# Kernel optimization log

Hardware: AMD Instinct MI355X
Metric: run time of the kernel (lower is better)

Reference implementation:

```python
import jax, jax.numpy as jnp
import numpy as np

N_NODES = 50000
N_EDGES = 600000
LATENT = 128
STEPS = 4
BN_EPS = 1e-5


def _bn(h, gamma, beta):
    # BatchNorm1d in training mode: batch statistics over the row dim (biased var)
    mean = jnp.mean(h, axis=0)
    var = jnp.var(h, axis=0)
    return gamma * (h - mean) * jax.lax.rsqrt(var + BN_EPS) + beta


def setup_inputs() -> dict:
    key = jax.random.key(0)
    ks = jax.random.split(key, 9)
    L, S = LATENT, STEPS
    d = {}
    d["x"] = jax.random.normal(ks[0], (N_NODES, L), dtype=jnp.float32)
    d["edge_attr"] = jax.random.normal(ks[1], (N_EDGES, L), dtype=jnp.float32)
    d["edge_index"] = jax.random.randint(ks[2], (2, N_EDGES), 0, N_NODES, dtype=jnp.int64)
    # MLP weights: small init (BN normalizes hidden activations anyway)
    d["edge_W1"] = jax.random.normal(ks[3], (S, 3 * L, L), dtype=jnp.float32) * (1.0 / np.sqrt(3 * L))
    d["edge_b1"] = jnp.zeros((S, L), jnp.float32)
    d["edge_g1"] = jnp.ones((S, L), jnp.float32)
    d["edge_be1"] = jnp.zeros((S, L), jnp.float32)
    d["edge_W2"] = jax.random.normal(ks[4], (S, L, L), dtype=jnp.float32) * (1.0 / np.sqrt(L))
    d["edge_b2"] = jnp.zeros((S, L), jnp.float32)
    d["node_W1"] = jax.random.normal(ks[5], (S, 2 * L, L), dtype=jnp.float32) * (1.0 / np.sqrt(2 * L))
    d["node_b1"] = jnp.zeros((S, L), jnp.float32)
    d["node_g1"] = jnp.ones((S, L), jnp.float32)
    d["node_be1"] = jnp.zeros((S, L), jnp.float32)
    d["node_W2"] = jax.random.normal(ks[6], (S, L, L), dtype=jnp.float32) * (1.0 / np.sqrt(L))
    d["node_b2"] = jnp.zeros((S, L), jnp.float32)
    return d


def reference(x, edge_attr, edge_index, edge_W1, edge_b1, edge_g1, edge_be1,
              edge_W2, edge_b2, node_W1, node_b1, node_g1, node_be1,
              node_W2, node_b2):
    src = edge_index[0]  # x_j (source)
    dst = edge_index[1]  # x_i (target), also the scatter target
    for s in range(STEPS):
        # --- edge update (message) ---
        m = jnp.concatenate([x[dst], x[src], edge_attr], axis=1)  # [E, 3L]
        h = _bn(m @ edge_W1[s] + edge_b1[s], edge_g1[s], edge_be1[s])
        h = jax.nn.relu(h)
        h = jax.nn.relu(h @ edge_W2[s] + edge_b2[s])
        edge_attr = h + edge_attr  # residual
        # --- aggregate: scatter-sum to target nodes ---
        agg = jax.ops.segment_sum(edge_attr, dst, num_segments=N_NODES)  # [N, L]
        # --- node update ---
        n = jnp.concatenate([x, agg], axis=1)  # [N, 2L]
        h = _bn(n @ node_W1[s] + node_b1[s], node_g1[s], node_be1[s])
        h = jax.nn.relu(h)
        h = jax.nn.relu(h @ node_W2[s] + node_b2[s])
        x = h + x  # residual
    return x, edge_attr
```

## Files before the change

### kernel.cpp

```cpp
#include <hip/hip_runtime.h>
#include <hip/hip_bf16.h>
#include <cstdint>
#include <cstddef>

#define E_N 600000
#define NND 50000
#define L 128

typedef unsigned short u16;
typedef unsigned int u32;
typedef __attribute__((ext_vector_type(8))) short bf16x8;
typedef __attribute__((ext_vector_type(4))) float f32x4;

static __device__ __forceinline__ u16 f2bf(float f) {
  union { float f; u32 u; } c; c.f = f;
  return (u16)((c.u + 0x7fffu + ((c.u >> 16) & 1u)) >> 16);
}
static __device__ __forceinline__ u32 pk2(float a, float b) {
  return (u32)f2bf(a) | ((u32)f2bf(b) << 16);
}
static __device__ __forceinline__ float bf2f(u32 h) {
  union { u32 u; float f; } c; c.u = (h & 0xffffu) << 16; return c.f;
}
static __device__ __forceinline__ void atomAddF(float* p, float v) {
#if defined(__HIP_DEVICE_COMPILE__)
  unsafeAtomicAdd(p, v);
#else
  atomicAdd(p, v);
#endif
}
static __device__ __forceinline__ bf16x8 pack8(float4 a, float4 b) {
  union { bf16x8 v; u32 w[4]; } r;
  r.w[0] = pk2(a.x, a.y); r.w[1] = pk2(a.z, a.w);
  r.w[2] = pk2(b.x, b.y); r.w[3] = pk2(b.z, b.w);
  return r.v;
}
static __device__ __forceinline__ bf16x8 bnrelu8(bf16x8 raw, float4 sca, float4 scb,
                                                 float4 sha, float4 shb) {
  union { bf16x8 v; u16 h[8]; } in; in.v = raw;
  const float sc[8] = {sca.x, sca.y, sca.z, sca.w, scb.x, scb.y, scb.z, scb.w};
  const float sh[8] = {sha.x, sha.y, sha.z, sha.w, shb.x, shb.y, shb.z, shb.w};
  float f[8];
  #pragma unroll
  for (int i = 0; i < 8; ++i) f[i] = fmaxf(bf2f(in.h[i]) * sc[i] + sh[i], 0.f);
  union { bf16x8 v; u32 w[4]; } r;
  #pragma unroll
  for (int i = 0; i < 4; ++i) r.w[i] = pk2(f[2 * i], f[2 * i + 1]);
  return r.v;
}

#define MFMA(a, bfr, c) __builtin_amdgcn_mfma_f32_16x16x32_bf16((a), (bfr), (c), 0, 0, 0)

struct Stg { uint4 v[4]; };
template <int KF>
static __device__ __forceinline__ void stageLoad(const u16* __restrict__ Wt, int kc, int tid, Stg& s) {
  #pragma unroll
  for (int i = 0; i < 4; ++i) {
    const int slot = tid + i * 256;
    const int n = slot >> 3, kq = slot & 7;
    s.v[i] = *(const uint4*)(Wt + (size_t)n * KF + kc * 64 + kq * 8);
  }
}
static __device__ __forceinline__ void stageWrite(char* BsB, int tid, const Stg& s) {
  #pragma unroll
  for (int i = 0; i < 4; ++i) {
    const int slot = tid + i * 256;
    const int n = slot >> 3, kq = slot & 7;
    *(uint4*)(BsB + ((n * 128 + kq * 16) ^ ((n & 7) << 4))) = s.v[i];
  }
}
static __device__ __forceinline__ void chunkMFMA(const char* BsB, int wc, int l15, int lq,
                                                 const bf16x8 (&af)[2][2], f32x4 (&acc)[2][4]) {
  #pragma unroll
  for (int k2 = 0; k2 < 2; ++k2) {
    #pragma unroll
    for (int n = 0; n < 4; ++n) {
      const int col = wc * 64 + n * 16 + l15;
      const bf16x8 bfr = *(const bf16x8*)(BsB + ((col * 128 + k2 * 64 + lq * 16) ^ ((col & 7) << 4)));
      acc[0][n] = MFMA(af[0][k2], bfr, acc[0][n]);
      acc[1][n] = MFMA(af[1][k2], bfr, acc[1][n]);
    }
  }
}

__global__ __launch_bounds__(256) void k_cvt4(const float* __restrict__ in,
                                              u16* __restrict__ out, int n4) {
  const int i = blockIdx.x * 256 + threadIdx.x;
  if (i < n4) {
    const float4 v = *(const float4*)(in + (size_t)i * 4);
    uint2 o; o.x = pk2(v.x, v.y); o.y = pk2(v.z, v.w);
    *(uint2*)(out + (size_t)i * 4) = o;
  }
}

__global__ void k_wt(const float* __restrict__ W, u16* __restrict__ Wt, int K) {
  const int idx = blockIdx.x * 256 + threadIdx.x;
  const int total = 4 * K * 128;
  if (idx >= total) return;
  const int s = idx / (K * 128);
  const int rem = idx - s * K * 128;
  const int n = rem / K;
  const int k = rem - n * K;
  Wt[idx] = f2bf(W[(size_t)s * K * 128 + (size_t)k * 128 + n]);
}

__global__ void k_hist(const int* __restrict__ dstI, int* __restrict__ cnt) {
  const int i = blockIdx.x * 256 + threadIdx.x;
  if (i < E_N) atomicAdd(&cnt[dstI[i]], 1);
}

__global__ __launch_bounds__(1024) void k_scan(const int* __restrict__ cnt, int* __restrict__ startA) {
  __shared__ int buf[1024];
  __shared__ int carry;
  const int tid = threadIdx.x;
  if (tid == 0) carry = 0;
  __syncthreads();
  for (int base = 0; base < NND; base += 1024) {
    int v = (base + tid < NND) ? cnt[base + tid] : 0;
    buf[tid] = v;
    __syncthreads();
    for (int off = 1; off < 1024; off <<= 1) {
      int t = (tid >= off) ? buf[tid - off] : 0;
      __syncthreads();
      buf[tid] += t;
      __syncthreads();
    }
    const int incl = buf[tid];
    const int c = carry;
    if (base + tid < NND) startA[base + tid] = c + incl - v;
    __syncthreads();
    if (tid == 1023) carry = c + incl;
    __syncthreads();
  }
  if (tid == 0) startA[NND] = carry;
}

__global__ void k_fill(const int* __restrict__ dstI, const int* __restrict__ startA,
                       int* __restrict__ cur, int* __restrict__ eids) {
  const int i = blockIdx.x * 256 + threadIdx.x;
  if (i < E_N) {
    const int d = dstI[i];
    const int pos = atomicAdd(&cur[d], 1);
    eids[startA[d] + pos] = i;
  }
}

__global__ void k_perm(const int* __restrict__ srcI, const int* __restrict__ dstI,
                       const int* __restrict__ perm,
                       int* __restrict__ srcP, int* __restrict__ dstP) {
  const int i = blockIdx.x * 256 + threadIdx.x;
  if (i < E_N) {
    const int e = perm[i];
    srcP[i] = srcI[e];
    dstP[i] = dstI[e];
  }
}

__global__ __launch_bounds__(256) void k_agg(const u16* __restrict__ ea16,
                                             const int* __restrict__ startA,
                                             u16* __restrict__ agg16) {
  const int node = blockIdx.x * 4 + (threadIdx.x >> 6);
  const int lane = threadIdx.x & 63;
  if (node >= NND) return;
  const int s = startA[node], e = startA[node + 1];
  float a0 = 0.f, a1 = 0.f, b0 = 0.f, b1 = 0.f;
  int i = s;
  for (; i + 1 < e; i += 2) {
    const u32 v0 = *(const u32*)(ea16 + (size_t)i * L + lane * 2);
    const u32 v1 = *(const u32*)(ea16 + (size_t)(i + 1) * L + lane * 2);
    a0 += bf2f(v0); a1 += bf2f(v0 >> 16);
    b0 += bf2f(v1); b1 += bf2f(v1 >> 16);
  }
  if (i < e) {
    const u32 v = *(const u32*)(ea16 + (size_t)i * L + lane * 2);
    a0 += bf2f(v); a1 += bf2f(v >> 16);
  }
  *(u32*)(agg16 + (size_t)node * L + lane * 2) = pk2(a0 + b0, a1 + b1);
}

__global__ void k_bnfin(const float* __restrict__ gS, const float* __restrict__ g,
                        const float* __restrict__ be, float invM, float* __restrict__ ss) {
  const int c = threadIdx.x;
  float s1 = 0.f, s2 = 0.f;
  for (int j = 0; j < 64; ++j) { s1 += gS[j * L + c]; s2 += gS[64 * L + j * L + c]; }
  const float mean = s1 * invM;
  const float var = s2 * invM - mean * mean;
  const float sc = g[c] * rsqrtf(var + 1e-5f);
  ss[c] = sc;
  ss[L + c] = be[c] - mean * sc;
}

template <bool EA32>
__global__ __launch_bounds__(256) void k_edge_l1(
    const u16* __restrict__ x16, const float* __restrict__ ea32,
    const u16* __restrict__ ea16, const int* __restrict__ perm,
    const int* __restrict__ srcP, const int* __restrict__ dstP,
    const u16* __restrict__ Wt, const float* __restrict__ b,
    u16* __restrict__ h1, float* __restrict__ gS)
{
  __shared__ char Bs[2][16384];
  __shared__ float red[256];
  const int tid = threadIdx.x, bid = blockIdx.x, row0 = bid * 64;
  red[tid] = 0.f;
  const int lane = tid & 63, wid = tid >> 6, wr = wid >> 1, wc = wid & 1;
  const int l15 = lane & 15, lq = lane >> 4;
  const int r0 = row0 + wr * 32 + l15, r1 = r0 + 16;
  const int d0 = dstP[r0], d1 = dstP[r1];
  const int s0 = srcP[r0], s1v = srcP[r1];

  const u16* dp0 = x16 + (size_t)d0 * L;
  const u16* dp1 = x16 + (size_t)d1 * L;
  const u16* sp0 = x16 + (size_t)s0 * L;
  const u16* sp1 = x16 + (size_t)s1v * L;

  bf16x8 aEa[2][2][2], aSrc[2][2][2];
  if (EA32) {
    const float* pE0 = ea32 + (size_t)perm[r0] * L;
    const float* pE1 = ea32 + (size_t)perm[r1] * L;
    #pragma unroll
    for (int c = 0; c < 2; ++c)
      #pragma unroll
      for (int k2 = 0; k2 < 2; ++k2) {
        const int off = c * 64 + k2 * 32 + lq * 8;
        aEa[c][0][k2] = pack8(*(const float4*)(pE0 + off), *(const float4*)(pE0 + off + 4));
        aEa[c][1][k2] = pack8(*(const float4*)(pE1 + off), *(const float4*)(pE1 + off + 4));
      }
  } else {
    const u16* pE0 = ea16 + (size_t)r0 * L;
    const u16* pE1 = ea16 + (size_t)r1 * L;
    #pragma unroll
    for (int c = 0; c < 2; ++c)
      #pragma unroll
      for (int k2 = 0; k2 < 2; ++k2) {
        const int off = c * 64 + k2 * 32 + lq * 8;
        aEa[c][0][k2] = *(const bf16x8*)(pE0 + off);
        aEa[c][1][k2] = *(const bf16x8*)(pE1 + off);
      }
  }
  #pragma unroll
  for (int c = 0; c < 2; ++c)
    #pragma unroll
    for (int k2 = 0; k2 < 2; ++k2) {
      const int off = c * 64 + k2 * 32 + lq * 8;
      aSrc[c][0][k2] = *(const bf16x8*)(sp0 + off);
      aSrc[c][1][k2] = *(const bf16x8*)(sp1 + off);
    }

  f32x4 acc[2][4];
  #pragma unroll
  for (int m = 0; m < 2; ++m)
    #pragma unroll
    for (int n = 0; n < 4; ++n) acc[m][n] = (f32x4){0.f, 0.f, 0.f, 0.f};

  const int kcMap[6] = {4, 5, 0, 1, 2, 3};
  Stg sg;
  stageLoad<384>(Wt, kcMap[0], tid, sg);
  stageWrite(Bs[0], tid, sg);
  __syncthreads();
  #pragma unroll
  for (int cc = 0; cc < 6; ++cc) {
    if (cc < 5) stageLoad<384>(Wt, kcMap[cc + 1], tid, sg);
    bf16x8 af[2][2];
    if (cc < 2) {
      #pragma unroll
      for (int m = 0; m < 2; ++m)
        #pragma unroll
        for (int k2 = 0; k2 < 2; ++k2) af[m][k2] = aEa[cc][m][k2];
    } else if (cc < 4) {
      const int c = cc - 2;
      #pragma unroll
      for (int k2 = 0; k2 < 2; ++k2) {
        const int off = c * 64 + k2 * 32 + lq * 8;
        af[0][k2] = *(const bf16x8*)(dp0 + off);
        af[1][k2] = *(const bf16x8*)(dp1 + off);
      }
    } else {
      #pragma unroll
      for (int m = 0; m < 2; ++m)
        #pragma unroll
        for (int k2 = 0; k2 < 2; ++k2) af[m][k2] = aSrc[cc - 4][m][k2];
    }
    chunkMFMA(Bs[cc & 1], wc, l15, lq, af, acc);
    if (cc < 5) stageWrite(Bs[(cc + 1) & 1], tid, sg);
    __syncthreads();
  }

  float bb[4], s1[4], s2[4];
  #pragma unroll
  for (int n = 0; n < 4; ++n) { bb[n] = b[wc * 64 + n * 16 + l15]; s1[n] = 0.f; s2[n] = 0.f; }
  #pragma unroll
  for (int m = 0; m < 2; ++m)
    #pragma unroll
    for (int n = 0; n < 4; ++n) {
      const int col = wc * 64 + n * 16 + l15;
      #pragma unroll
      for (int r = 0; r < 4; ++r) {
        const int row = row0 + wr * 32 + m * 16 + lq * 4 + r;
        const float o = acc[m][n][r] + bb[n];
        s1[n] += o; s2[n] += o * o;
        h1[(size_t)row * L + col] = f2bf(o);
      }
    }
  #pragma unroll
  for (int n = 0; n < 4; ++n) {
    const int col = wc * 64 + n * 16 + l15;
    atomAddF(&red[col], s1[n]);
    atomAddF(&red[128 + col], s2[n]);
  }
  __syncthreads();
  const int slot = (bid & 63) * L;
  if (tid < 128) atomAddF(&gS[slot + tid], red[tid]);
  else atomAddF(&gS[64 * L + slot + (tid - 128)], red[tid]);
}

template <bool EA32, bool WF32>
__global__ __launch_bounds__(256) void k_edge_l2(
    const u16* __restrict__ h1, const float* __restrict__ ss,
    const u16* __restrict__ Wt, const float* __restrict__ b,
    const float* __restrict__ resid32, const u16* __restrict__ resid16,
    const int* __restrict__ perm,
    float* __restrict__ ea_out, u16* __restrict__ ea16)
{
  __shared__ char Bs[2][16384];
  const int tid = threadIdx.x, bid = blockIdx.x, row0 = bid * 64;
  const int lane = tid & 63, wid = tid >> 6, wr = wid >> 1, wc = wid & 1;
  const int l15 = lane & 15, lq = lane >> 4;
  const int r0 = row0 + wr * 32 + l15, r1 = r0 + 16;
  const u16* a0 = h1 + (size_t)r0 * L + lq * 8;
  const u16* a1 = h1 + (size_t)r1 * L + lq * 8;

  f32x4 acc[2][4];
  #pragma unroll
  for (int m = 0; m < 2; ++m)
    #pragma unroll
    for (int n = 0; n < 4; ++n) acc[m][n] = (f32x4){0.f, 0.f, 0.f, 0.f};

  Stg sg0, sg1;
  stageLoad<128>(Wt, 0, tid, sg0);
  stageLoad<128>(Wt, 1, tid, sg1);
  bf16x8 raw[2][2][2];
  #pragma unroll
  for (int c = 0; c < 2; ++c)
    #pragma unroll
    for (int k2 = 0; k2 < 2; ++k2) {
      raw[c][0][k2] = *(const bf16x8*)(a0 + c * 64 + k2 * 32);
      raw[c][1][k2] = *(const bf16x8*)(a1 + c * 64 + k2 * 32);
    }
  stageWrite(Bs[0], tid, sg0);
  stageWrite(Bs[1], tid, sg1);
  __syncthreads();

  #pragma unroll
  for (int c = 0; c < 2; ++c) {
    bf16x8 af[2][2];
    #pragma unroll
    for (int k2 = 0; k2 < 2; ++k2) {
      const int kg = c * 64 + k2 * 32 + lq * 8;
      const float4 sca = *(const float4*)(ss + kg), scb = *(const float4*)(ss + kg + 4);
      const float4 sha = *(const float4*)(ss + 128 + kg), shb = *(const float4*)(ss + 128 + kg + 4);
      af[0][k2] = bnrelu8(raw[c][0][k2], sca, scb, sha, shb);
      af[1][k2] = bnrelu8(raw[c][1][k2], sca, scb, sha, shb);
    }
    chunkMFMA(Bs[c], wc, l15, lq, af, acc);
  }

  float bb[4];
  #pragma unroll
  for (int n = 0; n < 4; ++n) bb[n] = b[wc * 64 + n * 16 + l15];
  #pragma unroll
  for (int m = 0; m < 2; ++m)
    #pragma unroll
    for (int n = 0; n < 4; ++n) {
      const int col = wc * 64 + n * 16 + l15;
      #pragma unroll
      for (int r = 0; r < 4; ++r) {
        const int row = row0 + wr * 32 + m * 16 + lq * 4 + r;
        float rs;
        if (EA32) rs = resid32[(size_t)perm[row] * L + col];
        else      rs = bf2f(resid16[(size_t)row * L + col]);
        const float o = fmaxf(acc[m][n][r] + bb[n], 0.f) + rs;
        if (WF32) ea_out[(size_t)perm[row] * L + col] = o;
        ea16[(size_t)row * L + col] = f2bf(o);
      }
    }
}

__global__ __launch_bounds__(256) void k_node_l1(
    const u16* __restrict__ x16, const u16* __restrict__ agg16,
    const u16* __restrict__ Wt, const float* __restrict__ b,
    u16* __restrict__ h1, float* __restrict__ gS)
{
  __shared__ char Bs[2][16384];
  __shared__ float red[256];
  const int tid = threadIdx.x, bid = blockIdx.x, row0 = bid * 64;
  red[tid] = 0.f;
  const int lane = tid & 63, wid = tid >> 6, wr = wid >> 1, wc = wid & 1;
  const int l15 = lane & 15, lq = lane >> 4;
  const int r0 = row0 + wr * 32 + l15, r1 = r0 + 16;
  const int rr0 = min(r0, NND - 1), rr1 = min(r1, NND - 1);

  const u16* aP[2][2];
  aP[0][0] = x16 + (size_t)rr0 * L;  aP[1][0] = x16 + (size_t)rr1 * L;
  aP[0][1] = agg16 + (size_t)rr0 * L; aP[1][1] = agg16 + (size_t)rr1 * L;

  f32x4 acc[2][4];
  #pragma unroll
  for (int m = 0; m < 2; ++m)
    #pragma unroll
    for (int n = 0; n < 4; ++n) acc[m][n] = (f32x4){0.f, 0.f, 0.f, 0.f};

  auto loadA = [&](int c, bf16x8 (&af)[2][2]) {
    const int seg = c >> 1;
    const int base = (c & 1) * 64 + lq * 8;
    #pragma unroll
    for (int k2 = 0; k2 < 2; ++k2) {
      af[0][k2] = *(const bf16x8*)(aP[0][seg] + base + k2 * 32);
      af[1][k2] = *(const bf16x8*)(aP[1][seg] + base + k2 * 32);
    }
  };

  bf16x8 aCur[2][2], aNxt[2][2];
  Stg sg;
  loadA(0, aCur);
  stageLoad<256>(Wt, 0, tid, sg);
  stageWrite(Bs[0], tid, sg);
  __syncthreads();
  #pragma unroll
  for (int c = 0; c < 4; ++c) {
    if (c + 1 < 4) { loadA(c + 1, aNxt); stageLoad<256>(Wt, c + 1, tid, sg); }
    chunkMFMA(Bs[c & 1], wc, l15, lq, aCur, acc);
    if (c + 1 < 4) stageWrite(Bs[(c + 1) & 1], tid, sg);
    __syncthreads();
    #pragma unroll
    for (int m = 0; m < 2; ++m)
      #pragma unroll
      for (int k2 = 0; k2 < 2; ++k2) aCur[m][k2] = aNxt[m][k2];
  }

  float bb[4], s1[4], s2[4];
  #pragma unroll
  for (int n = 0; n < 4; ++n) { bb[n] = b[wc * 64 + n * 16 + l15]; s1[n] = 0.f; s2[n] = 0.f; }
  #pragma unroll
  for (int m = 0; m < 2; ++m)
    #pragma unroll
    for (int n = 0; n < 4; ++n) {
      const int col = wc * 64 + n * 16 + l15;
      #pragma unroll
      for (int r = 0; r < 4; ++r) {
        const int row = row0 + wr * 32 + m * 16 + lq * 4 + r;
        if (row < NND) {
          const float o = acc[m][n][r] + bb[n];
          s1[n] += o; s2[n] += o * o;
          h1[(size_t)row * L + col] = f2bf(o);
        }
      }
    }
  #pragma unroll
  for (int n = 0; n < 4; ++n) {
    const int col = wc * 64 + n * 16 + l15;
    atomAddF(&red[col], s1[n]);
    atomAddF(&red[128 + col], s2[n]);
  }
  __syncthreads();
  const int slot = (bid & 63) * L;
  if (tid < 128) atomAddF(&gS[slot + tid], red[tid]);
  else atomAddF(&gS[64 * L + slot + (tid - 128)], red[tid]);
}

__global__ __launch_bounds__(256) void k_node_l2(
    const u16* __restrict__ h1, const float* __restrict__ ss,
    const u16* __restrict__ Wt, const float* __restrict__ b,
    const float* __restrict__ resid, float* __restrict__ x_out,
    u16* __restrict__ x16)
{
  __shared__ char Bs[2][16384];
  const int tid = threadIdx.x, bid = blockIdx.x, row0 = bid * 64;
  const int lane = tid & 63, wid = tid >> 6, wr = wid >> 1, wc = wid & 1;
  const int l15 = lane & 15, lq = lane >> 4;
  const int r0 = row0 + wr * 32 + l15, r1 = r0 + 16;
  const int rr0 = min(r0, NND - 1), rr1 = min(r1, NND - 1);
  const u16* a0 = h1 + (size_t)rr0 * L + lq * 8;
  const u16* a1 = h1 + (size_t)rr1 * L + lq * 8;

  f32x4 acc[2][4];
  #pragma unroll
  for (int m = 0; m < 2; ++m)
    #pragma unroll
    for (int n = 0; n < 4; ++n) acc[m][n] = (f32x4){0.f, 0.f, 0.f, 0.f};

  Stg sg0, sg1;
  stageLoad<128>(Wt, 0, tid, sg0);
  stageLoad<128>(Wt, 1, tid, sg1);
  bf16x8 raw[2][2][2];
  #pragma unroll
  for (int c = 0; c < 2; ++c)
    #pragma unroll
    for (int k2 = 0; k2 < 2; ++k2) {
      raw[c][0][k2] = *(const bf16x8*)(a0 + c * 64 + k2 * 32);
      raw[c][1][k2] = *(const bf16x8*)(a1 + c * 64 + k2 * 32);
    }
  stageWrite(Bs[0], tid, sg0);
  stageWrite(Bs[1], tid, sg1);
  __syncthreads();

  #pragma unroll
  for (int c = 0; c < 2; ++c) {
    bf16x8 af[2][2];
    #pragma unroll
    for (int k2 = 0; k2 < 2; ++k2) {
      const int kg = c * 64 + k2 * 32 + lq * 8;
      const float4 sca = *(const float4*)(ss + kg), scb = *(const float4*)(ss + kg + 4);
      const float4 sha = *(const float4*)(ss + 128 + kg), shb = *(const float4*)(ss + 128 + kg + 4);
      af[0][k2] = bnrelu8(raw[c][0][k2], sca, scb, sha, shb);
      af[1][k2] = bnrelu8(raw[c][1][k2], sca, scb, sha, shb);
    }
    chunkMFMA(Bs[c], wc, l15, lq, af, acc);
  }

  float bb[4];
  #pragma unroll
  for (int n = 0; n < 4; ++n) bb[n] = b[wc * 64 + n * 16 + l15];
  #pragma unroll
  for (int m = 0; m < 2; ++m)
    #pragma unroll
    for (int n = 0; n < 4; ++n) {
      const int col = wc * 64 + n * 16 + l15;
      #pragma unroll
      for (int r = 0; r < 4; ++r) {
        const int row = row0 + wr * 32 + m * 16 + lq * 4 + r;
        if (row < NND) {
          const float o = fmaxf(acc[m][n][r] + bb[n], 0.f) + resid[(size_t)row * L + col];
          x_out[(size_t)row * L + col] = o;
          x16[(size_t)row * L + col] = f2bf(o);
        }
      }
    }
}

extern "C" void kernel_launch(void* const* d_in, const int* in_sizes, int n_in,
                              void* d_out, int out_size, void* d_ws, size_t ws_size,
                              hipStream_t stream) {
  (void)in_sizes; (void)n_in; (void)out_size; (void)ws_size;
  const float* in_x  = (const float*)d_in[0];
  const float* in_ea = (const float*)d_in[1];
  const int*   ei    = (const int*)d_in[2];
  const float* eW1 = (const float*)d_in[3];
  const float* eb1 = (const float*)d_in[4];
  const float* eg1 = (const float*)d_in[5];
  const float* ebe1= (const float*)d_in[6];
  const float* eW2 = (const float*)d_in[7];
  const float* eb2 = (const float*)d_in[8];
  const float* nW1 = (const float*)d_in[9];
  const float* nb1 = (const float*)d_in[10];
  const float* ng1 = (const float*)d_in[11];
  const float* nbe1= (const float*)d_in[12];
  const float* nW2 = (const float*)d_in[13];
  const float* nb2 = (const float*)d_in[14];

  float* x  = (float*)d_out;
  float* ea = (float*)d_out + (size_t)NND * L;

  char* w = (char*)d_ws;
  u16* h1e  = (u16*)w;   w += (size_t)E_N * L * sizeof(u16);
  u16* ea16 = (u16*)w;   w += (size_t)E_N * L * sizeof(u16);
  u16* h1n  = (u16*)w;   w += (size_t)NND * L * sizeof(u16);
  u16* x16  = (u16*)w;   w += (size_t)NND * L * sizeof(u16);
  u16* agg16= (u16*)w;   w += (size_t)NND * L * sizeof(u16);
  float* gS  = (float*)w; w += (size_t)2 * 64 * L * sizeof(float);
  float* ss  = (float*)w; w += 4096;
  u16* eW1t = (u16*)w;   w += (size_t)4 * 128 * 384 * sizeof(u16);
  u16* eW2t = (u16*)w;   w += (size_t)4 * 128 * 128 * sizeof(u16);
  u16* nW1t = (u16*)w;   w += (size_t)4 * 128 * 256 * sizeof(u16);
  u16* nW2t = (u16*)w;   w += (size_t)4 * 128 * 128 * sizeof(u16);
  int* cnt    = (int*)w; w += (size_t)NND * sizeof(int);
  int* cur    = (int*)w; w += (size_t)NND * sizeof(int);
  int* startA = (int*)w; w += (size_t)(NND + 64) * sizeof(int);
  int* eids   = (int*)w; w += (size_t)E_N * sizeof(int);
  int* srcP   = (int*)w; w += (size_t)E_N * sizeof(int);
  int* dstP   = (int*)w; w += (size_t)E_N * sizeof(int);

  const int* srcI = ei;
  const int* dstI = ei + E_N;

  k_cvt4<<<(NND * L / 4 + 255) / 256, 256, 0, stream>>>(in_x, x16, NND * L / 4);
  k_wt<<<(4 * 384 * 128 + 255) / 256, 256, 0, stream>>>(eW1, eW1t, 384);
  k_wt<<<(4 * 128 * 128 + 255) / 256, 256, 0, stream>>>(eW2, eW2t, 128);
  k_wt<<<(4 * 256 * 128 + 255) / 256, 256, 0, stream>>>(nW1, nW1t, 256);
  k_wt<<<(4 * 128 * 128 + 255) / 256, 256, 0, stream>>>(nW2, nW2t, 128);
  hipMemsetAsync(cnt, 0, (size_t)NND * sizeof(int), stream);
  hipMemsetAsync(cur, 0, (size_t)NND * sizeof(int), stream);
  k_hist<<<(E_N + 255) / 256, 256, 0, stream>>>(dstI, cnt);
  k_scan<<<1, 1024, 0, stream>>>(cnt, startA);
  k_fill<<<(E_N + 255) / 256, 256, 0, stream>>>(dstI, startA, cur, eids);
  k_perm<<<(E_N + 255) / 256, 256, 0, stream>>>(srcI, dstI, eids, srcP, dstP);

  const int egrid = E_N / 64;
  const int ngrid = (NND + 63) / 64;

  for (int s = 0; s < 4; ++s) {
    hipMemsetAsync(gS, 0, (size_t)2 * 64 * L * sizeof(float), stream);
    if (s == 0)
      k_edge_l1<true><<<egrid, 256, 0, stream>>>(x16, in_ea, nullptr, eids, srcP, dstP,
          eW1t + (size_t)s * 128 * 384, eb1 + (size_t)s * L, h1e, gS);
    else
      k_edge_l1<false><<<egrid, 256, 0, stream>>>(x16, nullptr, ea16, eids, srcP, dstP,
          eW1t + (size_t)s * 128 * 384, eb1 + (size_t)s * L, h1e, gS);
    k_bnfin<<<1, 128, 0, stream>>>(gS, eg1 + (size_t)s * L, ebe1 + (size_t)s * L,
        1.f / (float)E_N, ss);
    if (s == 0)
      k_edge_l2<true, false><<<egrid, 256, 0, stream>>>(h1e, ss,
          eW2t + (size_t)s * 128 * 128, eb2 + (size_t)s * L, in_ea, nullptr, eids, ea, ea16);
    else if (s < 3)
      k_edge_l2<false, false><<<egrid, 256, 0, stream>>>(h1e, ss,
          eW2t + (size_t)s * 128 * 128, eb2 + (size_t)s * L, nullptr, ea16, eids, ea, ea16);
    else
      k_edge_l2<false, true><<<egrid, 256, 0, stream>>>(h1e, ss,
          eW2t + (size_t)s * 128 * 128, eb2 + (size_t)s * L, nullptr, ea16, eids, ea, ea16);
    k_agg<<<(NND + 3) / 4, 256, 0, stream>>>(ea16, startA, agg16);
    hipMemsetAsync(gS, 0, (size_t)2 * 64 * L * sizeof(float), stream);
    k_node_l1<<<ngrid, 256, 0, stream>>>(x16, agg16,
        nW1t + (size_t)s * 128 * 256, nb1 + (size_t)s * L, h1n, gS);
    k_bnfin<<<1, 128, 0, stream>>>(gS, ng1 + (size_t)s * L, nbe1 + (size_t)s * L,
        1.f / (float)NND, ss);
    k_node_l2<<<ngrid, 256, 0, stream>>>(h1n, ss,
        nW2t + (size_t)s * 128 * 128, nb2 + (size_t)s * L,
        (s == 0) ? in_x : x, x, x16);
  }
}
```

Baseline: 2.264 ms.

## Use 512-thread edge blocks and stage edge outputs through LDS for coalesced stores

The edge layer-1 and layer-2 kernels now run 512 threads over 128 edge rows per block, so each staged weight tile in shared memory serves twice as many rows. Partial last blocks are handled by clamping row indices and guarding the statistics and stores. The epilogues write bf16 results into a swizzled shared-memory tile, then each thread emits full 16-byte row segments, with the residual add done at that point. This is meant to replace scattered 2-byte global stores and residual reads with coalesced vector accesses. The cost is extra barriers, a larger register and LDS footprint per block, and possibly lower occupancy.

Result: slower. 2.335 ms (+3.1%).

```diff
diff --git a/kernel.cpp b/kernel.cpp
--- a/kernel.cpp
+++ b/kernel.cpp
@@ -51,9 +51,27 @@
 
 #define MFMA(a, bfr, c) __builtin_amdgcn_mfma_f32_16x16x32_bf16((a), (bfr), (c), 0, 0, 0)
 
-struct Stg { uint4 v[4]; };
+struct Stg2 { uint4 v[2]; };
 template <int KF>
-static __device__ __forceinline__ void stageLoad(const u16* __restrict__ Wt, int kc, int tid, Stg& s) {
+static __device__ __forceinline__ void stageLoad2(const u16* __restrict__ Wt, int kc, int tid, Stg2& s) {
+  #pragma unroll
+  for (int i = 0; i < 2; ++i) {
+    const int slot = tid + i * 512;
+    const int n = slot >> 3, kq = slot & 7;
+    s.v[i] = *(const uint4*)(Wt + (size_t)n * KF + kc * 64 + kq * 8);
+  }
+}
+static __device__ __forceinline__ void stageWrite2(char* BsB, int tid, const Stg2& s) {
+  #pragma unroll
+  for (int i = 0; i < 2; ++i) {
+    const int slot = tid + i * 512;
+    const int n = slot >> 3, kq = slot & 7;
+    *(uint4*)(BsB + ((n * 128 + kq * 16) ^ ((n & 7) << 4))) = s.v[i];
+  }
+}
+struct Stg4 { uint4 v[4]; };
+template <int KF>
+static __device__ __forceinline__ void stageLoad4(const u16* __restrict__ Wt, int kc, int tid, Stg4& s) {
   #pragma unroll
   for (int i = 0; i < 4; ++i) {
     const int slot = tid + i * 256;
@@ -61,7 +79,7 @@
     s.v[i] = *(const uint4*)(Wt + (size_t)n * KF + kc * 64 + kq * 8);
   }
 }
-static __device__ __forceinline__ void stageWrite(char* BsB, int tid, const Stg& s) {
+static __device__ __forceinline__ void stageWrite4(char* BsB, int tid, const Stg4& s) {
   #pragma unroll
   for (int i = 0; i < 4; ++i) {
     const int slot = tid + i * 256;
@@ -191,7 +209,7 @@
 }
 
 template <bool EA32>
-__global__ __launch_bounds__(256) void k_edge_l1(
+__global__ __launch_bounds__(512, 5) void k_edge_l1(
     const u16* __restrict__ x16, const float* __restrict__ ea32,
     const u16* __restrict__ ea16, const int* __restrict__ perm,
     const int* __restrict__ srcP, const int* __restrict__ dstP,
@@ -200,13 +218,15 @@
 {
   __shared__ char Bs[2][16384];
   __shared__ float red[256];
-  const int tid = threadIdx.x, bid = blockIdx.x, row0 = bid * 64;
-  red[tid] = 0.f;
-  const int lane = tid & 63, wid = tid >> 6, wr = wid >> 1, wc = wid & 1;
+  const int tid = threadIdx.x, bid = blockIdx.x, row0 = bid * 128;
+  if (tid < 256) red[tid] = 0.f;
+  const int lane = tid & 63, wid = tid >> 6;
+  const int wr = wid >> 1, wc = wid & 1;
   const int l15 = lane & 15, lq = lane >> 4;
   const int r0 = row0 + wr * 32 + l15, r1 = r0 + 16;
-  const int d0 = dstP[r0], d1 = dstP[r1];
-  const int s0 = srcP[r0], s1v = srcP[r1];
+  const int cr0 = min(r0, E_N - 1), cr1 = min(r1, E_N - 1);
+  const int d0 = dstP[cr0], d1 = dstP[cr1];
+  const int s0 = srcP[cr0], s1v = srcP[cr1];
 
   const u16* dp0 = x16 + (size_t)d0 * L;
   const u16* dp1 = x16 + (size_t)d1 * L;
@@ -215,8 +235,8 @@
 
   bf16x8 aEa[2][2][2], aSrc[2][2][2];
   if (EA32) {
-    const float* pE0 = ea32 + (size_t)perm[r0] * L;
-    const float* pE1 = ea32 + (size_t)perm[r1] * L;
+    const float* pE0 = ea32 + (size_t)perm[cr0] * L;
+    const float* pE1 = ea32 + (size_t)perm[cr1] * L;
     #pragma unroll
     for (int c = 0; c < 2; ++c)
       #pragma unroll
@@ -226,8 +246,8 @@
         aEa[c][1][k2] = pack8(*(const float4*)(pE1 + off), *(const float4*)(pE1 + off + 4));
       }
   } else {
-    const u16* pE0 = ea16 + (size_t)r0 * L;
-    const u16* pE1 = ea16 + (size_t)r1 * L;
+    const u16* pE0 = ea16 + (size_t)cr0 * L;
+    const u16* pE1 = ea16 + (size_t)cr1 * L;
     #pragma unroll
     for (int c = 0; c < 2; ++c)
       #pragma unroll
@@ -253,13 +273,13 @@
     for (int n = 0; n < 4; ++n) acc[m][n] = (f32x4){0.f, 0.f, 0.f, 0.f};
 
   const int kcMap[6] = {4, 5, 0, 1, 2, 3};
-  Stg sg;
-  stageLoad<384>(Wt, kcMap[0], tid, sg);
-  stageWrite(Bs[0], tid, sg);
+  Stg2 sg;
+  stageLoad2<384>(Wt, kcMap[0], tid, sg);
+  stageWrite2(Bs[0], tid, sg);
   __syncthreads();
   #pragma unroll
   for (int cc = 0; cc < 6; ++cc) {
-    if (cc < 5) stageLoad<384>(Wt, kcMap[cc + 1], tid, sg);
+    if (cc < 5) stageLoad2<384>(Wt, kcMap[cc + 1], tid, sg);
     bf16x8 af[2][2];
     if (cc < 2) {
       #pragma unroll
@@ -281,13 +301,14 @@
         for (int k2 = 0; k2 < 2; ++k2) af[m][k2] = aSrc[cc - 4][m][k2];
     }
     chunkMFMA(Bs[cc & 1], wc, l15, lq, af, acc);
-    if (cc < 5) stageWrite(Bs[(cc + 1) & 1], tid, sg);
+    if (cc < 5) stageWrite2(Bs[(cc + 1) & 1], tid, sg);
     __syncthreads();
   }
 
-  float bb[4], s1[4], s2[4];
-  #pragma unroll
-  for (int n = 0; n < 4; ++n) { bb[n] = b[wc * 64 + n * 16 + l15]; s1[n] = 0.f; s2[n] = 0.f; }
+  float bb[4], s1[4] = {0.f,0.f,0.f,0.f}, s2[4] = {0.f,0.f,0.f,0.f};
+  #pragma unroll
+  for (int n = 0; n < 4; ++n) bb[n] = b[wc * 64 + n * 16 + l15];
+  char* T = (char*)Bs;
   #pragma unroll
   for (int m = 0; m < 2; ++m)
     #pragma unroll
@@ -295,26 +316,42 @@
       const int col = wc * 64 + n * 16 + l15;
       #pragma unroll
       for (int r = 0; r < 4; ++r) {
-        const int row = row0 + wr * 32 + m * 16 + lq * 4 + r;
+        const int rl = wr * 32 + m * 16 + lq * 4 + r;
         const float o = acc[m][n][r] + bb[n];
-        s1[n] += o; s2[n] += o * o;
-        h1[(size_t)row * L + col] = f2bf(o);
+        const int byte = (rl * 256 + col * 2) ^ (((rl >> 2) & 7) << 4);
+        *(u16*)(T + byte) = f2bf(o);
+        if (row0 + rl < E_N) { s1[n] += o; s2[n] += o * o; }
       }
     }
+  __syncthreads();
   #pragma unroll
   for (int n = 0; n < 4; ++n) {
     const int col = wc * 64 + n * 16 + l15;
     atomAddF(&red[col], s1[n]);
     atomAddF(&red[128 + col], s2[n]);
   }
+  {
+    const int rr = tid >> 2, qq = tid & 3;
+    const int grow = row0 + rr;
+    if (grow < E_N) {
+      const int rsw = ((rr >> 2) & 7) << 4;
+      uint4 o[4];
+      #pragma unroll
+      for (int j = 0; j < 4; ++j)
+        o[j] = *(const uint4*)(T + ((rr * 256 + j * 64 + qq * 16) ^ rsw));
+      u16* dp = h1 + (size_t)grow * L + qq * 8;
+      #pragma unroll
+      for (int j = 0; j < 4; ++j) *(uint4*)(dp + j * 32) = o[j];
+    }
+  }
   __syncthreads();
   const int slot = (bid & 63) * L;
   if (tid < 128) atomAddF(&gS[slot + tid], red[tid]);
-  else atomAddF(&gS[64 * L + slot + (tid - 128)], red[tid]);
+  else if (tid < 256) atomAddF(&gS[64 * L + slot + (tid - 128)], red[tid]);
 }
 
 template <bool EA32, bool WF32>
-__global__ __launch_bounds__(256) void k_edge_l2(
+__global__ __launch_bounds__(512, 5) void k_edge_l2(
     const u16* __restrict__ h1, const float* __restrict__ ss,
     const u16* __restrict__ Wt, const float* __restrict__ b,
     const float* __restrict__ resid32, const u16* __restrict__ resid16,
@@ -322,12 +359,14 @@
     float* __restrict__ ea_out, u16* __restrict__ ea16)
 {
   __shared__ char Bs[2][16384];
-  const int tid = threadIdx.x, bid = blockIdx.x, row0 = bid * 64;
-  const int lane = tid & 63, wid = tid >> 6, wr = wid >> 1, wc = wid & 1;
+  const int tid = threadIdx.x, bid = blockIdx.x, row0 = bid * 128;
+  const int lane = tid & 63, wid = tid >> 6;
+  const int wr = wid >> 1, wc = wid & 1;
   const int l15 = lane & 15, lq = lane >> 4;
   const int r0 = row0 + wr * 32 + l15, r1 = r0 + 16;
-  const u16* a0 = h1 + (size_t)r0 * L + lq * 8;
-  const u16* a1 = h1 + (size_t)r1 * L + lq * 8;
+  const int cr0 = min(r0, E_N - 1), cr1 = min(r1, E_N - 1);
+  const u16* a0 = h1 + (size_t)cr0 * L + lq * 8;
+  const u16* a1 = h1 + (size_t)cr1 * L + lq * 8;
 
   f32x4 acc[2][4];
   #pragma unroll
@@ -335,9 +374,9 @@
     #pragma unroll
     for (int n = 0; n < 4; ++n) acc[m][n] = (f32x4){0.f, 0.f, 0.f, 0.f};
 
-  Stg sg0, sg1;
-  stageLoad<128>(Wt, 0, tid, sg0);
-  stageLoad<128>(Wt, 1, tid, sg1);
+  Stg2 sg0, sg1;
+  stageLoad2<128>(Wt, 0, tid, sg0);
+  stageLoad2<128>(Wt, 1, tid, sg1);
   bf16x8 raw[2][2][2];
   #pragma unroll
   for (int c = 0; c < 2; ++c)
@@ -346,8 +385,8 @@
       raw[c][0][k2] = *(const bf16x8*)(a0 + c * 64 + k2 * 32);
       raw[c][1][k2] = *(const bf16x8*)(a1 + c * 64 + k2 * 32);
     }
-  stageWrite(Bs[0], tid, sg0);
-  stageWrite(Bs[1], tid, sg1);
+  stageWrite2(Bs[0], tid, sg0);
+  stageWrite2(Bs[1], tid, sg1);
   __syncthreads();
 
   #pragma unroll
@@ -363,10 +402,12 @@
     }
     chunkMFMA(Bs[c], wc, l15, lq, af, acc);
   }
+  __syncthreads();
 
   float bb[4];
   #pragma unroll
   for (int n = 0; n < 4; ++n) bb[n] = b[wc * 64 + n * 16 + l15];
+  char* T = (char*)Bs;
   #pragma unroll
   for (int m = 0; m < 2; ++m)
     #pragma unroll
@@ -374,15 +415,65 @@
       const int col = wc * 64 + n * 16 + l15;
       #pragma unroll
       for (int r = 0; r < 4; ++r) {
-        const int row = row0 + wr * 32 + m * 16 + lq * 4 + r;
-        float rs;
-        if (EA32) rs = resid32[(size_t)perm[row] * L + col];
-        else      rs = bf2f(resid16[(size_t)row * L + col]);
-        const float o = fmaxf(acc[m][n][r] + bb[n], 0.f) + rs;
-        if (WF32) ea_out[(size_t)perm[row] * L + col] = o;
-        ea16[(size_t)row * L + col] = f2bf(o);
+        const int rl = wr * 32 + m * 16 + lq * 4 + r;
+        const float o = fmaxf(acc[m][n][r] + bb[n], 0.f);
+        const int byte = (rl * 256 + col * 2) ^ (((rl >> 2) & 7) << 4);
+        *(u16*)(T + byte) = f2bf(o);
       }
     }
+  __syncthreads();
+  {
+    const int rr = tid >> 2, qq = tid & 3;
+    const int grow = row0 + rr;
+    if (grow < E_N) {
+      const int rsw = ((rr >> 2) & 7) << 4;
+      uint4 h[4];
+      #pragma unroll
+      for (int j = 0; j < 4; ++j)
+        h[j] = *(const uint4*)(T + ((rr * 256 + j * 64 + qq * 16) ^ rsw));
+      u16* dp16 = ea16 + (size_t)grow * L + qq * 8;
+      if (EA32) {
+        const float* rp = resid32 + (size_t)perm[grow] * L + qq * 8;
+        #pragma unroll
+        for (int j = 0; j < 4; ++j) {
+          const float4 ra = *(const float4*)(rp + j * 32);
+          const float4 rb = *(const float4*)(rp + j * 32 + 4);
+          const u32* hw = (const u32*)&h[j];
+          uint4 ov;
+          ov.x = pk2(bf2f(hw[0]) + ra.x, bf2f(hw[0] >> 16) + ra.y);
+          ov.y = pk2(bf2f(hw[1]) + ra.z, bf2f(hw[1] >> 16) + ra.w);
+          ov.z = pk2(bf2f(hw[2]) + rb.x, bf2f(hw[2] >> 16) + rb.y);
+          ov.w = pk2(bf2f(hw[3]) + rb.z, bf2f(hw[3] >> 16) + rb.w);
+          *(uint4*)(dp16 + j * 32) = ov;
+        }
+      } else {
+        const u16* rp = resid16 + (size_t)grow * L + qq * 8;
+        float* fp = WF32 ? (ea_out + (size_t)perm[grow] * L + qq * 8) : nullptr;
+        #pragma unroll
+        for (int j = 0; j < 4; ++j) {
+          const uint4 rv = *(const uint4*)(rp + j * 32);
+          const u32* hw = (const u32*)&h[j];
+          const u32* rw = (const u32*)&rv;
+          float f[8];
+          #pragma unroll
+          for (int w2 = 0; w2 < 4; ++w2) {
+            f[2 * w2]     = bf2f(hw[w2])       + bf2f(rw[w2]);
+            f[2 * w2 + 1] = bf2f(hw[w2] >> 16) + bf2f(rw[w2] >> 16);
+          }
+          uint4 ov;
+          ov.x = pk2(f[0], f[1]); ov.y = pk2(f[2], f[3]);
+          ov.z = pk2(f[4], f[5]); ov.w = pk2(f[6], f[7]);
+          *(uint4*)(dp16 + j * 32) = ov;
+          if (WF32) {
+            float4 fa; fa.x = f[0]; fa.y = f[1]; fa.z = f[2]; fa.w = f[3];
+            float4 fb; fb.x = f[4]; fb.y = f[5]; fb.z = f[6]; fb.w = f[7];
+            *(float4*)(fp + j * 32) = fa;
+            *(float4*)(fp + j * 32 + 4) = fb;
+          }
+        }
+      }
+    }
+  }
 }
 
 __global__ __launch_bounds__(256) void k_node_l1(
@@ -420,16 +511,16 @@
   };
 
   bf16x8 aCur[2][2], aNxt[2][2];
-  Stg sg;
+  Stg4 sg;
   loadA(0, aCur);
-  stageLoad<256>(Wt, 0, tid, sg);
-  stageWrite(Bs[0], tid, sg);
+  stageLoad4<256>(Wt, 0, tid, sg);
+  stageWrite4(Bs[0], tid, sg);
   __syncthreads();
   #pragma unroll
   for (int c = 0; c < 4; ++c) {
-    if (c + 1 < 4) { loadA(c + 1, aNxt); stageLoad<256>(Wt, c + 1, tid, sg); }
+    if (c + 1 < 4) { loadA(c + 1, aNxt); stageLoad4<256>(Wt, c + 1, tid, sg); }
     chunkMFMA(Bs[c & 1], wc, l15, lq, aCur, acc);
-    if (c + 1 < 4) stageWrite(Bs[(c + 1) & 1], tid, sg);
+    if (c + 1 < 4) stageWrite4(Bs[(c + 1) & 1], tid, sg);
     __syncthreads();
     #pragma unroll
     for (int m = 0; m < 2; ++m)
@@ -488,9 +579,11 @@
     #pragma unroll
     for (int n = 0; n < 4; ++n) acc[m][n] = (f32x4){0.f, 0.f, 0.f, 0.f};
 
-  Stg sg0, sg1;
-  stageLoad<128>(Wt, 0, tid, sg0);
-  stageLoad<128>(Wt, 1, tid, sg1);
+  Stg2 sg0, sg1;
+  stageLoad2<128>(Wt, 0, tid & 255, sg0);
+  Stg4 sg0b, sg1b;
+  stageLoad4<128>(Wt, 0, tid, sg0b);
+  stageLoad4<128>(Wt, 1, tid, sg1b);
   bf16x8 raw[2][2][2];
   #pragma unroll
   for (int c = 0; c < 2; ++c)
@@ -499,8 +592,8 @@
       raw[c][0][k2] = *(const bf16x8*)(a0 + c * 64 + k2 * 32);
       raw[c][1][k2] = *(const bf16x8*)(a1 + c * 64 + k2 * 32);
     }
-  stageWrite(Bs[0], tid, sg0);
-  stageWrite(Bs[1], tid, sg1);
+  stageWrite4(Bs[0], tid, sg0b);
+  stageWrite4(Bs[1], tid, sg1b);
   __syncthreads();
 
   #pragma unroll
@@ -594,27 +687,27 @@
   k_fill<<<(E_N + 255) / 256, 256, 0, stream>>>(dstI, startA, cur, eids);
   k_perm<<<(E_N + 255) / 256, 256, 0, stream>>>(srcI, dstI, eids, srcP, dstP);
 
-  const int egrid = E_N / 64;
+  const int egrid = (E_N + 127) / 128;
   const int ngrid = (NND + 63) / 64;
 
   for (int s = 0; s < 4; ++s) {
     hipMemsetAsync(gS, 0, (size_t)2 * 64 * L * sizeof(float), stream);
     if (s == 0)
-      k_edge_l1<true><<<egrid, 256, 0, stream>>>(x16, in_ea, nullptr, eids, srcP, dstP,
+      k_edge_l1<true><<<egrid, 512, 0, stream>>>(x16, in_ea, nullptr, eids, srcP, dstP,
           eW1t + (size_t)s * 128 * 384, eb1 + (size_t)s * L, h1e, gS);
     else
-      k_edge_l1<false><<<egrid, 256, 0, stream>>>(x16, nullptr, ea16, eids, srcP, dstP,
+      k_edge_l1<false><<<egrid, 512, 0, stream>>>(x16, nullptr, ea16, eids, srcP, dstP,
           eW1t + (size_t)s * 128 * 384, eb1 + (size_t)s * L, h1e, gS);
     k_bnfin<<<1, 128, 0, stream>>>(gS, eg1 + (size_t)s * L, ebe1 + (size_t)s * L,
         1.f / (float)E_N, ss);
     if (s == 0)
-      k_edge_l2<true, false><<<egrid, 256, 0, stream>>>(h1e, ss,
+      k_edge_l2<true, false><<<egrid, 512, 0, stream>>>(h1e, ss,
           eW2t + (size_t)s * 128 * 128, eb2 + (size_t)s * L, in_ea, nullptr, eids, ea, ea16);
     else if (s < 3)
-      k_edge_l2<false, false><<<egrid, 256, 0, stream>>>(h1e, ss,
+      k_edge_l2<false, false><<<egrid, 512, 0, stream>>>(h1e, ss,
           eW2t + (size_t)s * 128 * 128, eb2 + (size_t)s * L, nullptr, ea16, eids, ea, ea16);
     else
-      k_edge_l2<false, true><<<egrid, 256, 0, stream>>>(h1e, ss,
+      k_edge_l2<false, true><<<egrid, 512, 0, stream>>>(h1e, ss,
           eW2t + (size_t)s * 128 * 128, eb2 + (size_t)s * L, nullptr, ea16, eids, ea, ea16);
     k_agg<<<(NND + 3) / 4, 256, 0, stream>>>(ea16, startA, agg16);
     hipMemsetAsync(gS, 0, (size_t)2 * 64 * L * sizeof(float), stream);
```
